# Performance work log

Measured on AMD Instinct MI355X. Metric: run time of the kernel, lower is better.

The kernel has to match this reference:

```python
import jax, jax.numpy as jnp
import numpy as np
import math

B, H, W, CV = 8, 128, 128, 256
T, CT = 77, 512
HEADS, HEAD_DIM = 8, 32
TOP_M = 5
LN_EPS = 1e-5
NORM_EPS = 1e-6
CLAMP = 2.0


def _ln(x, w, b):
    mu = jnp.mean(x, axis=-1, keepdims=True)
    var = jnp.mean(jnp.square(x - mu), axis=-1, keepdims=True)
    return (x - mu) * jax.lax.rsqrt(var + LN_EPS) * w + b


def _l2norm(x):
    n = jnp.sqrt(jnp.sum(jnp.square(x), axis=-1, keepdims=True))
    return x / jnp.maximum(n, NORM_EPS)


def setup_inputs() -> dict:
    key = jax.random.key(0)
    ks = jax.random.split(key, 12)
    s = 0.02
    return {
        "visual_features": jax.random.normal(ks[0], (B, H, W, CV), jnp.float32),
        "text_features": jax.random.normal(ks[1], (B, T, CT), jnp.float32),
        "norm1_w": jnp.ones((CV,), jnp.float32),
        "norm1_b": jnp.zeros((CV,), jnp.float32),
        "q_w": s * jax.random.normal(ks[2], (CV, CV), jnp.float32),
        "q_b": jnp.zeros((CV,), jnp.float32),
        "k_w": s * jax.random.normal(ks[3], (CT, CV), jnp.float32),
        "k_b": jnp.zeros((CV,), jnp.float32),
        "v_w": s * jax.random.normal(ks[4], (CT, CV), jnp.float32),
        "v_b": jnp.zeros((CV,), jnp.float32),
        "out_w": s * jax.random.normal(ks[5], (CV, CV), jnp.float32),
        "out_b": jnp.zeros((CV,), jnp.float32),
        "gate_w": s * jax.random.normal(ks[6], (CV, 1), jnp.float32),
        "gate_b": jnp.zeros((1,), jnp.float32),
        "logit_scale": jnp.asarray(math.log(1.0 / 0.07), jnp.float32),
        "alpha": jnp.asarray(0.1, jnp.float32),
        "norm2_w": jnp.ones((CV,), jnp.float32),
        "norm2_b": jnp.zeros((CV,), jnp.float32),
        "ffn1_w": s * jax.random.normal(ks[7], (CV, 4 * CV), jnp.float32),
        "ffn1_b": jnp.zeros((4 * CV,), jnp.float32),
        "ffn2_w": s * jax.random.normal(ks[8], (4 * CV, CV), jnp.float32),
        "ffn2_b": jnp.zeros((CV,), jnp.float32),
    }


def reference(visual_features, text_features, norm1_w, norm1_b, q_w, q_b, k_w, k_b,
              v_w, v_b, out_w, out_b, gate_w, gate_b, logit_scale, alpha,
              norm2_w, norm2_b, ffn1_w, ffn1_b, ffn2_w, ffn2_b):
    b, h, w, cv = visual_features.shape
    n = h * w
    # Pre-LN then flatten spatial dims: (B, N, Cv)
    x = _ln(visual_features, norm1_w, norm1_b).reshape(b, n, cv)
    q_full = x @ q_w + q_b                      # (B, N, Cv)
    k_full = text_features @ k_w + k_b          # (B, T, Cv)
    v_full = text_features @ v_w + v_b          # (B, T, Cv)
    # padding mask: all-zero text tokens
    pad = jnp.sum(jnp.abs(text_features), axis=-1) <= 1e-6  # (B, T)
    # cosine-normalize over FULL Cv dim, then split heads
    q = _l2norm(q_full).reshape(b, n, HEADS, HEAD_DIM)
    k = _l2norm(k_full).reshape(b, -1, HEADS, HEAD_DIM)
    v = v_full.reshape(b, -1, HEADS, HEAD_DIM)
    scale = jnp.exp(jnp.clip(logit_scale, -CLAMP, CLAMP)) / jnp.sqrt(jnp.float32(HEAD_DIM))
    sim = jnp.einsum('bnhd,bthd->bnht', q, k) * scale  # (B, N, Hh, T)
    sim = jnp.where(pad[:, None, None, :], -jnp.inf, sim)
    # top-k pruning over text tokens (threshold at k-th value; ties measure-zero)
    topv = jax.lax.top_k(sim, TOP_M)[0]
    sim = jnp.where(sim >= topv[..., -1:], sim, -jnp.inf)
    attn = jax.nn.softmax(sim, axis=-1)
    aligned = jnp.einsum('bnht,bthd->bnhd', attn, v).reshape(b, n, cv)
    aligned = aligned @ out_w + out_b
    gate = jax.nn.sigmoid(x @ gate_w + gate_b)  # (B, N, 1)
    y = x + alpha * gate * aligned
    y = _ln(y, norm2_w, norm2_b)
    ffn = jax.nn.gelu(y @ ffn1_w + ffn1_b, approximate=False) @ ffn2_w + ffn2_b
    y = y + ffn
    return y.reshape(b, h, w, cv)
```

## Files before the change

### kernel.cpp

```cpp
#include <hip/hip_runtime.h>
#include <hip/hip_bf16.h>

typedef _Float16 h16;
typedef __attribute__((ext_vector_type(8))) _Float16 halfx8;
typedef __attribute__((ext_vector_type(4))) _Float16 halfx4;
typedef __attribute__((ext_vector_type(4))) float f32x4;

__device__ __forceinline__ void gload_lds16(const void* g, void* l) {
  __builtin_amdgcn_global_load_lds((const __attribute__((address_space(1))) unsigned int*)g,
                                   (__attribute__((address_space(3))) unsigned int*)l, 16, 0, 0);
}
__device__ __forceinline__ unsigned umax_(unsigned a, unsigned b) { return a > b ? a : b; }
__device__ __forceinline__ unsigned umin_(unsigned a, unsigned b) { return a < b ? a : b; }

__device__ __forceinline__ float fast_gelu(float v) {
  float x2 = v * v;
  float w_ = v * fmaf(x2, 0.0713548163f, 1.5957691216f);
  float e = __expf(w_);
  float r = 1.f / (1.f + e);
  return v * e * r;
}

__global__ __launch_bounds__(256) void prep_kernel(
    const float* __restrict__ tf, const float* __restrict__ kw, const float* __restrict__ kb,
    const float* __restrict__ vw, const float* __restrict__ vb, const float* __restrict__ lsp,
    h16* __restrict__ ko, h16* __restrict__ vo, float* __restrict__ padf,
    const float* __restrict__ qw, const float* __restrict__ ow,
    const float* __restrict__ f1w, const float* __restrict__ f2w,
    h16* __restrict__ qwT, h16* __restrict__ owT,
    h16* __restrict__ f1T, h16* __restrict__ f2T,
    const float* __restrict__ vis, const float* __restrict__ n1w, const float* __restrict__ n1b,
    const float* __restrict__ gw, const float* __restrict__ gb,
    h16* __restrict__ x, float* __restrict__ gate)
{
  __shared__ h16 st[4 * 512];
  __shared__ float kro[4 * 256];
  __shared__ float ssc[4];
  int bid = blockIdx.x, tid = threadIdx.x;
  int lane = tid & 63, wid = tid >> 6;

  if (bid < 160) {
    int b = bid / 20, tg = bid % 20, t0 = tg * 4;
    for (int i = tid; i < 4 * 512; i += 256) {
      int tl = i >> 9, j = i & 511, t = t0 + tl;
      float v = (t < 77) ? tf[((size_t)b * 77 + t) * 512 + j] : 0.f;
      st[i] = (h16)v;
    }
    __syncthreads();
    {
      int t = t0 + wid;
      float a = 0.f;
      #pragma unroll
      for (int j = 0; j < 8; j++) a += fabsf((float)st[wid * 512 + lane + j * 64]);
      #pragma unroll
      for (int o = 32; o; o >>= 1) a += __shfl_xor(a, o);
      if (lane == 0) padf[b * 80 + t] = (a <= 1e-6f) ? -1e30f : 0.f;
    }
    int c = tid;
    float kacc[4], vacc[4];
    #pragma unroll
    for (int tl = 0; tl < 4; tl++) { kacc[tl] = kb[c]; vacc[tl] = vb[c]; }
    for (int j = 0; j < 512; j++) {
      float wkv = kw[(size_t)j * 256 + c];
      float wvv = vw[(size_t)j * 256 + c];
      #pragma unroll
      for (int tl = 0; tl < 4; tl++) {
        float xv = (float)st[tl * 512 + j];
        kacc[tl] += xv * wkv; vacc[tl] += xv * wvv;
      }
    }
    #pragma unroll
    for (int tl = 0; tl < 4; tl++) kro[tl * 256 + c] = kacc[tl] * kacc[tl];
    __syncthreads();
    {
      float s2 = kro[wid * 256 + lane] + kro[wid * 256 + lane + 64]
               + kro[wid * 256 + lane + 128] + kro[wid * 256 + lane + 192];
      #pragma unroll
      for (int o = 32; o; o >>= 1) s2 += __shfl_xor(s2, o);
      if (lane == 0) {
        float ls = lsp[0];
        float scale = __expf(fminf(fmaxf(ls, -2.f), 2.f)) * rsqrtf(32.f);
        ssc[wid] = scale / fmaxf(sqrtf(s2), 1e-6f);
      }
    }
    __syncthreads();
    int h = c >> 5, d = c & 31, g = d >> 3, e = d & 7;
    #pragma unroll
    for (int tl = 0; tl < 4; tl++) {
      int t = t0 + tl;
      int kt = t >> 4, l15 = t & 15, ln = g * 16 + l15;
      size_t koff = ((((size_t)(b * 8 + h) * 5 + kt) * 64) + ln) * 8 + e;
      size_t voff = (((size_t)(b * 8 + h) * 80) + t) * 32 + d;
      ko[koff] = (t < 77) ? (h16)(kacc[tl] * ssc[tl]) : (h16)0.f;
      vo[voff] = (t < 77) ? (h16)vacc[tl] : (h16)0.f;
    }
  } else if (bid < 2720) {
    int cb = bid - 160;
    const float* in; h16* out; int logN, K, base;
    if (cb < 256)       { in = qw;  out = qwT; logN = 8;  K = 256;  base = 0; }
    else if (cb < 512)  { in = ow;  out = owT; logN = 8;  K = 256;  base = 256; }
    else if (cb < 1536) { in = f1w; out = f1T; logN = 10; K = 256;  base = 512; }
    else                { in = f2w; out = f2T; logN = 8;  K = 1024; base = 1536; }
    int idx = (cb - base) * 256 + tid;
    int k = idx >> logN, n = idx & ((1 << logN) - 1);
    out[(size_t)n * K + k] = (h16)in[idx];
  } else {
    size_t row = (size_t)(bid - 2720) * 4 + wid;
    const float4 v = ((const float4*)(vis + row * 256))[lane];
    float s = v.x + v.y + v.z + v.w;
    float q = v.x * v.x + v.y * v.y + v.z * v.z + v.w * v.w;
    #pragma unroll
    for (int o = 32; o; o >>= 1) { s += __shfl_xor(s, o); q += __shfl_xor(q, o); }
    float mean = s * (1.f / 256.f);
    float rstd = rsqrtf(q * (1.f / 256.f) - mean * mean + 1e-5f);
    float4 wv = ((const float4*)n1w)[lane], bv = ((const float4*)n1b)[lane];
    float x0 = (v.x - mean) * rstd * wv.x + bv.x;
    float x1 = (v.y - mean) * rstd * wv.y + bv.y;
    float x2 = (v.z - mean) * rstd * wv.z + bv.z;
    float x3 = (v.w - mean) * rstd * wv.w + bv.w;
    float4 gv = ((const float4*)gw)[lane];
    float g = x0 * gv.x + x1 * gv.y + x2 * gv.z + x3 * gv.w;
    #pragma unroll
    for (int o = 32; o; o >>= 1) g += __shfl_xor(g, o);
    if (lane == 0) gate[row] = 1.f / (1.f + __expf(-(g + gb[0])));
    halfx4 o4; o4[0] = (h16)x0; o4[1] = (h16)x1; o4[2] = (h16)x2; o4[3] = (h16)x3;
    ((halfx4*)(x + row * 256))[lane] = o4;
  }
}

__global__ __launch_bounds__(256) void gemmQA_kernel(const h16* __restrict__ A,
    const h16* __restrict__ Wt, const float* __restrict__ bias,
    const h16* __restrict__ kk,
    const h16* __restrict__ vv,
    const float* __restrict__ padf,
    h16* __restrict__ outp)
{
  __shared__ char sA[8192];
  __shared__ char sB[32768];
  int m0 = blockIdx.x * 64;
  int tid = threadIdx.x, lane = tid & 63, wid = tid >> 6;
  int wn = wid;
  int l15 = lane & 15, l4 = lane >> 4, xk = l15 & 7;
  f32x4 acc[4][4];
  #pragma unroll
  for (int a = 0; a < 4; a++)
    #pragma unroll
    for (int b2 = 0; b2 < 4; b2++) acc[a][b2] = (f32x4){0.f, 0.f, 0.f, 0.f};
  const size_t sa = 512;
  int srow = lane >> 3;
  int scol = ((lane & 7) ^ srow) * 16;
  const char* Ab = (const char*)A + (size_t)m0 * sa + scol;
  const char* Bb = (const char*)Wt + scol;
  for (int k0 = 0; k0 < 256; k0 += 64) {
    #pragma unroll
    for (int cc = 0; cc < 2; cc++) {
      int ch = wid * 2 + cc;
      gload_lds16(Ab + (size_t)(ch * 8 + srow) * sa + k0 * 2, sA + ch * 1024);
    }
    #pragma unroll
    for (int cc = 0; cc < 8; cc++) {
      int ch = wid * 8 + cc;
      gload_lds16(Bb + (size_t)(ch * 8 + srow) * sa + k0 * 2, sB + ch * 1024);
    }
    asm volatile("s_waitcnt vmcnt(0)" ::: "memory");
    __syncthreads();
    #pragma unroll
    for (int ks = 0; ks < 2; ks++) {
      halfx8 af[4], bf[4];
      #pragma unroll
      for (int f = 0; f < 4; f++) {
        af[f] = *(const halfx8*)(sA + (f * 16 + l15) * 128 + (((ks * 4 + l4) ^ xk) * 16));
        bf[f] = *(const halfx8*)(sB + (wn * 64 + f * 16 + l15) * 128 + (((ks * 4 + l4) ^ xk) * 16));
      }
      #pragma unroll
      for (int fm = 0; fm < 4; fm++)
        #pragma unroll
        for (int fn = 0; fn < 4; fn++)
          acc[fm][fn] = __builtin_amdgcn_mfma_f32_16x16x32_f16(af[fm], bf[fn], acc[fm][fn], 0, 0, 0);
    }
    __syncthreads();
  }
  float bv[4];
  #pragma unroll
  for (int fn = 0; fn < 4; fn++) bv[fn] = bias[wn * 64 + fn * 16 + l15];
  float ps[4][4];
  #pragma unroll
  for (int fm = 0; fm < 4; fm++)
    #pragma unroll
    for (int r = 0; r < 4; r++) {
      float s = 0.f;
      #pragma unroll
      for (int fn = 0; fn < 4; fn++) {
        float v = acc[fm][fn][r] + bv[fn];
        acc[fm][fn][r] = v;
        s += v * v;
      }
      ps[fm][r] = s;
    }
  #pragma unroll
  for (int o = 1; o <= 8; o <<= 1)
    #pragma unroll
    for (int fm = 0; fm < 4; fm++)
      #pragma unroll
      for (int r = 0; r < 4; r++) ps[fm][r] += __shfl_xor(ps[fm][r], o);
  if (l15 == 0) {
    #pragma unroll
    for (int fm = 0; fm < 4; fm++)
      #pragma unroll
      for (int r = 0; r < 4; r++)
        ((float*)sA)[(fm * 16 + l4 * 4 + r) * 4 + wn] = ps[fm][r];
  }
  __syncthreads();
  #pragma unroll
  for (int fm = 0; fm < 4; fm++)
    #pragma unroll
    for (int r = 0; r < 4; r++) {
      const float* p = (const float*)sA + (fm * 16 + l4 * 4 + r) * 4;
      float S = p[0] + p[1] + p[2] + p[3];
      float sc = 1.f / fmaxf(sqrtf(S), 1e-6f);
      int row = fm * 16 + l4 * 4 + r;
      #pragma unroll
      for (int fn = 0; fn < 4; fn++) {
        int col = wn * 64 + fn * 16 + l15;
        ((h16*)(sB + row * 512 + (((col >> 3) ^ (row & 7)) * 16)))[col & 7] =
            (h16)(acc[fm][fn][r] * sc);
      }
    }
  __syncthreads();

  {
    int bx = blockIdx.x;
    int g = l4;
    int b = bx >> 8;
    size_t qrow = (size_t)bx * 64 + wid * 16 + l15;
    int base4 = g * 4;
    float pad4[5][4];
    #pragma unroll
    for (int kt = 0; kt < 5; kt++) {
      float4 p4 = *(const float4*)&padf[b * 80 + kt * 16 + base4];
      pad4[kt][0] = p4.x; pad4[kt][1] = p4.y; pad4[kt][2] = p4.z; pad4[kt][3] = p4.w;
    }
    const char* qsrc = sB + (wid * 16 + l15) * 512;
    int rk = l15 & 7;
    h16* op = &outp[qrow * 256 + g * 8];
    #pragma unroll 2
    for (int h = 0; h < 8; h++) {
      int ho = h * 32;
      halfx8 qf = *(const halfx8*)(qsrc + (((h * 4 + l4) ^ rk) * 16));
      const h16* kph = kk + (((size_t)(b * 8 + h) * 5) * 64 + lane) * 8;
      const h16* vph = vv + ((size_t)(b * 8 + h) * 80) * 32 + g * 8;
      f32x4 acc5[5];
      #pragma unroll
      for (int kt = 0; kt < 5; kt++) {
        halfx8 kf = *(const halfx8*)(kph + kt * 512);
        acc5[kt] = __builtin_amdgcn_mfma_f32_16x16x32_f16(kf, qf, (f32x4){0.f, 0.f, 0.f, 0.f}, 0, 0, 0);
      }
      unsigned pv0 = 0u, pv1 = 0u, pv2 = 0u, pv3 = 0u, pv4 = 0u;
      #pragma unroll
      for (int kt = 0; kt < 5; kt++) {
        #pragma unroll
        for (int r = 0; r < 4; r++) {
          float s = acc5[kt][r] + pad4[kt][r];
          int bi = __float_as_int(s);
          unsigned u = ((unsigned)(bi ^ ((bi >> 31) | (int)0x80000000)) & 0xFFFFFF80u)
                     | (unsigned)(base4 + kt * 16 + r);
          unsigned a;
          a = umax_(pv0, u); u = umin_(pv0, u); pv0 = a;
          a = umax_(pv1, u); u = umin_(pv1, u); pv1 = a;
          a = umax_(pv2, u); u = umin_(pv2, u); pv2 = a;
          a = umax_(pv3, u); u = umin_(pv3, u); pv3 = a;
          pv4 = umax_(pv4, u);
        }
      }
      #pragma unroll
      for (int mrd = 0; mrd < 2; mrd++) {
        int msk = mrd ? 32 : 16;
        unsigned b0 = (unsigned)__shfl_xor((int)pv0, msk);
        unsigned b1 = (unsigned)__shfl_xor((int)pv1, msk);
        unsigned b2 = (unsigned)__shfl_xor((int)pv2, msk);
        unsigned b3 = (unsigned)__shfl_xor((int)pv3, msk);
        unsigned b4 = (unsigned)__shfl_xor((int)pv4, msk);
        unsigned c0 = umax_(pv0, b0);
        unsigned c1 = umax_(umax_(umin_(pv0, b0), pv1), b1);
        unsigned c2 = umax_(umax_(umin_(pv0, b1), umin_(pv1, b0)), umax_(pv2, b2));
        unsigned c3 = umax_(umax_(umax_(umin_(pv0, b2), umin_(pv1, b1)), umin_(pv2, b0)), umax_(pv3, b3));
        unsigned c4 = umax_(umax_(umax_(umin_(pv0, b3), umin_(pv1, b2)),
                                  umax_(umin_(pv2, b1), umin_(pv3, b0))), umax_(pv4, b4));
        pv0 = c0; pv1 = c1; pv2 = c2; pv3 = c3; pv4 = c4;
      }
      unsigned pvs[5] = {pv0, pv1, pv2, pv3, pv4};
      float pw[5]; int ti[5]; float den = 0.f;
      #pragma unroll
      for (int k = 0; k < 5; k++) {
        unsigned u = pvs[k];
        int sg = ((int)u) >> 31;
        float tv = __int_as_float(u ^ (0x80000000u | (unsigned)~sg));
        ti[k] = (int)(u & 0x7Fu);
        pw[k] = __expf(tv);
        den += pw[k];
      }
      float inv = 1.f / den;
      halfx8 o8 = {};
      #pragma unroll
      for (int k = 0; k < 5; k++) {
        h16 ph = (h16)(pw[k] * inv);
        halfx8 v = *(const halfx8*)(vph + ti[k] * 32);
        halfx8 p8 = {ph, ph, ph, ph, ph, ph, ph, ph};
        o8 = o8 + p8 * v;
      }
      *(halfx8*)(op + ho) = o8;
    }
  }
}

__global__ __launch_bounds__(256) void gemmO_kernel(const h16* __restrict__ A,
    const h16* __restrict__ Wt, const float* __restrict__ ob,
    const h16* __restrict__ x, const float* __restrict__ gate,
    const float* __restrict__ alphap, const float* __restrict__ w2,
    const float* __restrict__ b2, h16* __restrict__ outp)
{
  __shared__ char sA[8192];
  __shared__ char sB[32768];
  int m0 = blockIdx.x * 64;
  int tid = threadIdx.x, lane = tid & 63, wid = tid >> 6;
  int wn = wid;
  int l15 = lane & 15, l4 = lane >> 4, xk = l15 & 7;
  f32x4 acc[4][4];
  #pragma unroll
  for (int a = 0; a < 4; a++)
    #pragma unroll
    for (int b2_ = 0; b2_ < 4; b2_++) acc[a][b2_] = (f32x4){0.f, 0.f, 0.f, 0.f};
  const size_t sa = 512;
  int srow = lane >> 3;
  int scol = ((lane & 7) ^ srow) * 16;
  const char* Ab = (const char*)A + (size_t)m0 * sa + scol;
  const char* Bb = (const char*)Wt + scol;
  for (int k0 = 0; k0 < 256; k0 += 64) {
    #pragma unroll
    for (int cc = 0; cc < 2; cc++) {
      int ch = wid * 2 + cc;
      gload_lds16(Ab + (size_t)(ch * 8 + srow) * sa + k0 * 2, sA + ch * 1024);
    }
    #pragma unroll
    for (int cc = 0; cc < 8; cc++) {
      int ch = wid * 8 + cc;
      gload_lds16(Bb + (size_t)(ch * 8 + srow) * sa + k0 * 2, sB + ch * 1024);
    }
    asm volatile("s_waitcnt vmcnt(0)" ::: "memory");
    __syncthreads();
    #pragma unroll
    for (int ks = 0; ks < 2; ks++) {
      halfx8 af[4], bf[4];
      #pragma unroll
      for (int f = 0; f < 4; f++) {
        af[f] = *(const halfx8*)(sA + (f * 16 + l15) * 128 + (((ks * 4 + l4) ^ xk) * 16));
        bf[f] = *(const halfx8*)(sB + (wn * 64 + f * 16 + l15) * 128 + (((ks * 4 + l4) ^ xk) * 16));
      }
      #pragma unroll
      for (int fm = 0; fm < 4; fm++)
        #pragma unroll
        for (int fn = 0; fn < 4; fn++)
          acc[fm][fn] = __builtin_amdgcn_mfma_f32_16x16x32_f16(af[fm], bf[fn], acc[fm][fn], 0, 0, 0);
    }
    __syncthreads();
  }
  float bv[4], w2v[4], b2v[4];
  #pragma unroll
  for (int fn = 0; fn < 4; fn++) {
    int col = wn * 64 + fn * 16 + l15;
    bv[fn] = ob[col]; w2v[fn] = w2[col]; b2v[fn] = b2[col];
  }
  float al = alphap[0];
  float s1[4][4], s2[4][4];
  #pragma unroll
  for (int fm = 0; fm < 4; fm++)
    #pragma unroll
    for (int r = 0; r < 4; r++) {
      size_t row = (size_t)(m0 + fm * 16 + l4 * 4 + r);
      float ga = al * gate[row];
      float a1 = 0.f, a2 = 0.f;
      #pragma unroll
      for (int fn = 0; fn < 4; fn++) {
        float v = acc[fm][fn][r] + bv[fn];
        float xv = (float)x[row * 256 + wn * 64 + fn * 16 + l15];
        float y = xv + ga * v;
        acc[fm][fn][r] = y;
        a1 += y; a2 += y * y;
      }
      s1[fm][r] = a1; s2[fm][r] = a2;
    }
  #pragma unroll
  for (int o = 1; o <= 8; o <<= 1)
    #pragma unroll
    for (int fm = 0; fm < 4; fm++)
      #pragma unroll
      for (int r = 0; r < 4; r++) {
        s1[fm][r] += __shfl_xor(s1[fm][r], o);
        s2[fm][r] += __shfl_xor(s2[fm][r], o);
      }
  if (l15 == 0) {
    #pragma unroll
    for (int fm = 0; fm < 4; fm++)
      #pragma unroll
      for (int r = 0; r < 4; r++) {
        int rr = fm * 16 + l4 * 4 + r;
        ((float*)sA)[rr * 8 + wn * 2 + 0] = s1[fm][r];
        ((float*)sA)[rr * 8 + wn * 2 + 1] = s2[fm][r];
      }
  }
  __syncthreads();
  #pragma unroll
  for (int fm = 0; fm < 4; fm++)
    #pragma unroll
    for (int r = 0; r < 4; r++) {
      int rr = fm * 16 + l4 * 4 + r;
      const float* p = (const float*)sA + rr * 8;
      float S1 = p[0] + p[2] + p[4] + p[6];
      float S2 = p[1] + p[3] + p[5] + p[7];
      float mean = S1 * (1.f / 256.f);
      float var = S2 * (1.f / 256.f) - mean * mean;
      float rstd = rsqrtf(var + 1e-5f);
      size_t row = (size_t)(m0 + rr);
      #pragma unroll
      for (int fn = 0; fn < 4; fn++) {
        float y = acc[fm][fn][r];
        outp[row * 256 + wn * 64 + fn * 16 + l15] =
            (h16)((y - mean) * rstd * w2v[fn] + b2v[fn]);
      }
    }
}

__device__ __forceinline__ void ffn_stage_w1(const h16* __restrict__ w1t,
                                             int c, char* dW1, int tid, int wid)
{
  #pragma unroll
  for (int j = 0; j < 4; j++) {
    int i = j * 512 + tid;
    int r = i >> 5, g = i & 31;
    gload_lds16(w1t + (size_t)(c * 64 + r) * 256 + ((g ^ (r & 7)) * 8),
                dW1 + (j * 512 + wid * 64) * 16);
  }
}
__device__ __forceinline__ void ffn_stage_w2(const h16* __restrict__ w2t,
                                             int c, char* dW2, int tid, int wid)
{
  #pragma unroll
  for (int j = 0; j < 4; j++) {
    int i = j * 512 + tid;
    int r = i >> 3, g = i & 7;
    gload_lds16(w2t + (size_t)r * 1024 + c * 64 + ((g ^ (r & 7)) * 8),
                dW2 + (j * 512 + wid * 64) * 16);
  }
}

__global__ __launch_bounds__(512, 2) void ffn_fused_kernel(
    const h16* __restrict__ y2g, const h16* __restrict__ w1t, const float* __restrict__ b1,
    const h16* __restrict__ w2t, const float* __restrict__ b2, float* __restrict__ outp)
{
  __shared__ char smem[163840];
  float* sE = (float*)smem;

  int m0 = blockIdx.x * 128;
  int tid = threadIdx.x, lane = tid & 63, wid = tid >> 6;
  int l15 = lane & 15, l4 = lane >> 4;
  int wm1 = wid >> 1, wn1 = wid & 1;
  int wm2 = wid >> 2, wn2 = wid & 3;

  halfx8 afy[2][8];
  #pragma unroll
  for (int fm = 0; fm < 2; fm++) {
    size_t row = (size_t)(m0 + wm1 * 32 + fm * 16 + l15);
    #pragma unroll
    for (int ks = 0; ks < 8; ks++)
      afy[fm][ks] = *(const halfx8*)&y2g[row * 256 + ks * 32 + l4 * 8];
  }

  f32x4 acc2[4][4];
  #pragma unroll
  for (int a = 0; a < 4; a++)
    #pragma unroll
    for (int b_ = 0; b_ < 4; b_++) acc2[a][b_] = (f32x4){0.f, 0.f, 0.f, 0.f};

  ffn_stage_w1(w1t, 0, smem, tid, wid);
  float4 b1v[2];
  b1v[0] = *(const float4*)&b1[wn1 * 32 + l4 * 4];
  b1v[1] = *(const float4*)&b1[wn1 * 32 + 16 + l4 * 4];
  asm volatile("s_waitcnt vmcnt(0)" ::: "memory");
  __builtin_amdgcn_s_barrier();
  asm volatile("" ::: "memory");

  for (int c = 0; c < 16; c++) {
    int buf = c & 1;
    char* sW1c = smem + buf * 32768;
    if (c < 15) ffn_stage_w1(w1t, c + 1, smem + (buf ^ 1) * 32768, tid, wid);
    ffn_stage_w2(w2t, c, smem + 65536 + buf * 32768, tid, wid);
    float4 nb0 = {0.f, 0.f, 0.f, 0.f}, nb1 = {0.f, 0.f, 0.f, 0.f};
    if (c < 15) {
      nb0 = *(const float4*)&b1[(c + 1) * 64 + wn1 * 32 + l4 * 4];
      nb1 = *(const float4*)&b1[(c + 1) * 64 + wn1 * 32 + 16 + l4 * 4];
    }

    f32x4 a1[2][2];
    #pragma unroll
    for (int a = 0; a < 2; a++)
      #pragma unroll
      for (int b_ = 0; b_ < 2; b_++) a1[a][b_] = (f32x4){0.f, 0.f, 0.f, 0.f};
    __builtin_amdgcn_s_setprio(1);
    #pragma unroll
    for (int ks = 0; ks < 8; ks++) {
      #pragma unroll
      for (int fc = 0; fc < 2; fc++) {
        int nrow = wn1 * 32 + fc * 16 + l15;
        halfx8 bf = *(const halfx8*)(sW1c + (size_t)nrow * 512 + (((ks * 4 + l4) ^ (nrow & 7)) * 16));
        #pragma unroll
        for (int fm = 0; fm < 2; fm++)
          a1[fm][fc] = __builtin_amdgcn_mfma_f32_16x16x32_f16(bf, afy[fm][ks], a1[fm][fc], 0, 0, 0);
      }
    }
    __builtin_amdgcn_s_setprio(0);

    {
      char* sHc = smem + 131072 + buf * 16384;
      #pragma unroll
      for (int fm = 0; fm < 2; fm++) {
        int row = wm1 * 32 + fm * 16 + l15;
        int sx = (row & 7) << 1;
        #pragma unroll
        for (int fc = 0; fc < 2; fc++) {
          int slot = wn1 * 8 + fc * 4 + l4;
          float4 bb = b1v[fc];
          halfx4 hv;
          hv[0] = (h16)fast_gelu(a1[fm][fc][0] + bb.x);
          hv[1] = (h16)fast_gelu(a1[fm][fc][1] + bb.y);
          hv[2] = (h16)fast_gelu(a1[fm][fc][2] + bb.z);
          hv[3] = (h16)fast_gelu(a1[fm][fc][3] + bb.w);
          *(halfx4*)(sHc + row * 128 + ((slot ^ sx) * 8)) = hv;
        }
      }
    }

    if (c > 0) {
      char* sHp = smem + 131072 + (buf ^ 1) * 16384;
      char* sW2p = smem + 65536 + (buf ^ 1) * 32768;
      __builtin_amdgcn_s_setprio(1);
      #pragma unroll
      for (int ks = 0; ks < 2; ks++) {
        halfx8 ah[4], bw[4];
        #pragma unroll
        for (int f = 0; f < 4; f++) {
          int hrow = wm2 * 64 + f * 16 + l15;
          ah[f] = *(const halfx8*)(sHp + hrow * 128 + (((ks * 8 + l4 * 2) ^ ((hrow & 7) << 1)) * 8));
          int wrow = wn2 * 64 + f * 16 + l15;
          bw[f] = *(const halfx8*)(sW2p + (size_t)wrow * 128 + (((ks * 4 + l4) ^ (wrow & 7)) * 16));
        }
        #pragma unroll
        for (int fm = 0; fm < 4; fm++)
          #pragma unroll
          for (int fn = 0; fn < 4; fn++)
            acc2[fm][fn] = __builtin_amdgcn_mfma_f32_16x16x32_f16(ah[fm], bw[fn], acc2[fm][fn], 0, 0, 0);
      }
      __builtin_amdgcn_s_setprio(0);
    }

    asm volatile("s_waitcnt lgkmcnt(0)" ::: "memory");
    asm volatile("s_waitcnt vmcnt(0)" ::: "memory");
    __builtin_amdgcn_s_barrier();
    asm volatile("" ::: "memory");
    b1v[0] = nb0; b1v[1] = nb1;
  }

  {
    char* sHp = smem + 131072 + 16384;
    char* sW2p = smem + 65536 + 32768;
    __builtin_amdgcn_s_setprio(1);
    #pragma unroll
    for (int ks = 0; ks < 2; ks++) {
      halfx8 ah[4], bw[4];
      #pragma unroll
      for (int f = 0; f < 4; f++) {
        int hrow = wm2 * 64 + f * 16 + l15;
        ah[f] = *(const halfx8*)(sHp + hrow * 128 + (((ks * 8 + l4 * 2) ^ ((hrow & 7) << 1)) * 8));
        int wrow = wn2 * 64 + f * 16 + l15;
        bw[f] = *(const halfx8*)(sW2p + (size_t)wrow * 128 + (((ks * 4 + l4) ^ (wrow & 7)) * 16));
      }
      #pragma unroll
      for (int fm = 0; fm < 4; fm++)
        #pragma unroll
        for (int fn = 0; fn < 4; fn++)
          acc2[fm][fn] = __builtin_amdgcn_mfma_f32_16x16x32_f16(ah[fm], bw[fn], acc2[fm][fn], 0, 0, 0);
    }
    __builtin_amdgcn_s_setprio(0);
  }

  int rowl = tid >> 3, cg = tid & 7;
  #pragma unroll
  for (int half = 0; half < 2; half++) {
    if (wm2 == half) {
      #pragma unroll
      for (int fm = 0; fm < 4; fm++)
        #pragma unroll
        for (int fn = 0; fn < 4; fn++)
          #pragma unroll
          for (int r = 0; r < 4; r++)
            sE[(fm * 16 + l4 * 4 + r) * 264 + wn2 * 64 + fn * 16 + l15] = acc2[fm][fn][r];
    }
    __syncthreads();
    size_t grow = (size_t)(m0 + half * 64 + rowl);
    #pragma unroll
    for (int k = 0; k < 8; k++) {
      int c0 = cg * 4 + k * 32;
      float4 v = *(float4*)&sE[rowl * 264 + c0];
      halfx4 rv = *(const halfx4*)&y2g[grow * 256 + c0];
      float4 bb = *(const float4*)&b2[c0];
      float4 o;
      o.x = v.x + (float)rv[0] + bb.x;
      o.y = v.y + (float)rv[1] + bb.y;
      o.z = v.z + (float)rv[2] + bb.z;
      o.w = v.w + (float)rv[3] + bb.w;
      *(float4*)&outp[grow * 256 + c0] = o;
    }
    __syncthreads();
  }
}

extern "C" void kernel_launch(void* const* d_in, const int* in_sizes, int n_in,
                              void* d_out, int out_size, void* d_ws, size_t ws_size,
                              hipStream_t stream)
{
  const float* vis = (const float*)d_in[0];
  const float* tf  = (const float*)d_in[1];
  const float* n1w = (const float*)d_in[2];
  const float* n1b = (const float*)d_in[3];
  const float* qw  = (const float*)d_in[4];
  const float* qb  = (const float*)d_in[5];
  const float* kw  = (const float*)d_in[6];
  const float* kb  = (const float*)d_in[7];
  const float* vw  = (const float*)d_in[8];
  const float* vb  = (const float*)d_in[9];
  const float* ow  = (const float*)d_in[10];
  const float* ob  = (const float*)d_in[11];
  const float* gw  = (const float*)d_in[12];
  const float* gb  = (const float*)d_in[13];
  const float* ls  = (const float*)d_in[14];
  const float* al  = (const float*)d_in[15];
  const float* n2w = (const float*)d_in[16];
  const float* n2b = (const float*)d_in[17];
  const float* f1w = (const float*)d_in[18];
  const float* f1b = (const float*)d_in[19];
  const float* f2w = (const float*)d_in[20];
  const float* f2b = (const float*)d_in[21];

  char* ws = (char*)d_ws;
  const size_t MB_ = 1024ull * 1024ull;
  h16*  kS   = (h16*)(ws + 0 * MB_);
  h16*  vS   = (h16*)(ws + 1 * MB_);
  float* padf = (float*)(ws + 2 * MB_);
  float* gate = (float*)(ws + 3 * MB_);
  h16*  qwT  = (h16*)(ws + 4 * MB_);
  h16*  owT  = (h16*)(ws + 5 * MB_);
  h16*  f1T  = (h16*)(ws + 6 * MB_);
  h16*  f2T  = (h16*)(ws + 7 * MB_);
  h16*  xh   = (h16*)(ws + 16 * MB_);
  h16*  qh   = (h16*)(ws + 80 * MB_);
  h16*  alg  = (h16*)(ws + 144 * MB_);

  prep_kernel<<<35488, 256, 0, stream>>>(
      tf, kw, kb, vw, vb, ls, kS, vS, padf,
      qw, ow, f1w, f2w, qwT, owT, f1T, f2T,
      vis, n1w, n1b, gw, gb, xh, gate);

  gemmQA_kernel<<<2048, 256, 0, stream>>>(xh, qwT, qb, kS, vS, padf, qh);

  gemmO_kernel<<<2048, 256, 0, stream>>>(qh, owT, ob, xh, gate, al, n2w, n2b, alg);

  ffn_fused_kernel<<<1024, 512, 0, stream>>>(alg, f1T, f1b, f2T, f2b, (float*)d_out);
}
```

Measured before the change: 478.6 us.

## Fuse Q-projection/attention kernel with output projection and LayerNorm kernel

Merges the Q GEMM + top-k attention kernel with the out-projection + gate residual + LN2 kernel into one launch. The per-head aligned outputs stay in registers (o8s) and are written into LDS as the A operand of the out-projection GEMM, so the intermediate aligned tensor never makes the round trip through global memory. This saves one launch and roughly 32 MB of fp16 traffic. The cost is higher register pressure from holding eight halfx8 values plus fully unrolling the head loop, which may reduce occupancy.

Result: slower. 490.5 us (+2.5%).

```diff
diff --git a/kernel.cpp b/kernel.cpp
--- a/kernel.cpp
+++ b/kernel.cpp
@@ -128,12 +128,16 @@
   }
 }
 
-__global__ __launch_bounds__(256) void gemmQA_kernel(const h16* __restrict__ A,
+__global__ __launch_bounds__(256) void gemmQAO_kernel(const h16* __restrict__ A,
     const h16* __restrict__ Wt, const float* __restrict__ bias,
     const h16* __restrict__ kk,
     const h16* __restrict__ vv,
     const float* __restrict__ padf,
-    h16* __restrict__ outp)
+    const h16* __restrict__ Ot,
+    const float* __restrict__ ob,
+    const h16* __restrict__ x, const float* __restrict__ gate,
+    const float* __restrict__ alphap, const float* __restrict__ w2,
+    const float* __restrict__ b2, h16* __restrict__ outp)
 {
   __shared__ char sA[8192];
   __shared__ char sB[32768];
@@ -145,7 +149,7 @@
   #pragma unroll
   for (int a = 0; a < 4; a++)
     #pragma unroll
-    for (int b2 = 0; b2 < 4; b2++) acc[a][b2] = (f32x4){0.f, 0.f, 0.f, 0.f};
+    for (int b2_ = 0; b2_ < 4; b2_++) acc[a][b2_] = (f32x4){0.f, 0.f, 0.f, 0.f};
   const size_t sa = 512;
   int srow = lane >> 3;
   int scol = ((lane & 7) ^ srow) * 16;
@@ -228,12 +232,10 @@
     }
   __syncthreads();
 
+  halfx8 o8s[8];
   {
-    int bx = blockIdx.x;
-    int g = l4;
-    int b = bx >> 8;
-    size_t qrow = (size_t)bx * 64 + wid * 16 + l15;
-    int base4 = g * 4;
+    int b = blockIdx.x >> 8;
+    int base4 = l4 * 4;
     float pad4[5][4];
     #pragma unroll
     for (int kt = 0; kt < 5; kt++) {
@@ -242,13 +244,11 @@
     }
     const char* qsrc = sB + (wid * 16 + l15) * 512;
     int rk = l15 & 7;
-    h16* op = &outp[qrow * 256 + g * 8];
-    #pragma unroll 2
+    #pragma unroll
     for (int h = 0; h < 8; h++) {
-      int ho = h * 32;
       halfx8 qf = *(const halfx8*)(qsrc + (((h * 4 + l4) ^ rk) * 16));
       const h16* kph = kk + (((size_t)(b * 8 + h) * 5) * 64 + lane) * 8;
-      const h16* vph = vv + ((size_t)(b * 8 + h) * 80) * 32 + g * 8;
+      const h16* vph = vv + ((size_t)(b * 8 + h) * 80) * 32 + l4 * 8;
       f32x4 acc5[5];
       #pragma unroll
       for (int kt = 0; kt < 5; kt++) {
@@ -277,14 +277,14 @@
         int msk = mrd ? 32 : 16;
         unsigned b0 = (unsigned)__shfl_xor((int)pv0, msk);
         unsigned b1 = (unsigned)__shfl_xor((int)pv1, msk);
-        unsigned b2 = (unsigned)__shfl_xor((int)pv2, msk);
+        unsigned b2_ = (unsigned)__shfl_xor((int)pv2, msk);
         unsigned b3 = (unsigned)__shfl_xor((int)pv3, msk);
         unsigned b4 = (unsigned)__shfl_xor((int)pv4, msk);
         unsigned c0 = umax_(pv0, b0);
         unsigned c1 = umax_(umax_(umin_(pv0, b0), pv1), b1);
-        unsigned c2 = umax_(umax_(umin_(pv0, b1), umin_(pv1, b0)), umax_(pv2, b2));
-        unsigned c3 = umax_(umax_(umax_(umin_(pv0, b2), umin_(pv1, b1)), umin_(pv2, b0)), umax_(pv3, b3));
-        unsigned c4 = umax_(umax_(umax_(umin_(pv0, b3), umin_(pv1, b2)),
+        unsigned c2 = umax_(umax_(umin_(pv0, b1), umin_(pv1, b0)), umax_(pv2, b2_));
+        unsigned c3 = umax_(umax_(umax_(umin_(pv0, b2_), umin_(pv1, b1)), umin_(pv2, b0)), umax_(pv3, b3));
+        unsigned c4 = umax_(umax_(umax_(umin_(pv0, b3), umin_(pv1, b2_)),
                                   umax_(umin_(pv2, b1), umin_(pv3, b0))), umax_(pv4, b4));
         pv0 = c0; pv1 = c1; pv2 = c2; pv3 = c3; pv4 = c4;
       }
@@ -308,67 +308,58 @@
         halfx8 p8 = {ph, ph, ph, ph, ph, ph, ph, ph};
         o8 = o8 + p8 * v;
       }
-      *(halfx8*)(op + ho) = o8;
-    }
-  }
-}
-
-__global__ __launch_bounds__(256) void gemmO_kernel(const h16* __restrict__ A,
-    const h16* __restrict__ Wt, const float* __restrict__ ob,
-    const h16* __restrict__ x, const float* __restrict__ gate,
-    const float* __restrict__ alphap, const float* __restrict__ w2,
-    const float* __restrict__ b2, h16* __restrict__ outp)
-{
-  __shared__ char sA[8192];
-  __shared__ char sB[32768];
-  int m0 = blockIdx.x * 64;
-  int tid = threadIdx.x, lane = tid & 63, wid = tid >> 6;
-  int wn = wid;
-  int l15 = lane & 15, l4 = lane >> 4, xk = l15 & 7;
-  f32x4 acc[4][4];
+      o8s[h] = o8;
+    }
+  }
+
+  asm volatile("" ::: "memory");
+  __builtin_amdgcn_s_barrier();
+  asm volatile("" ::: "memory");
+
+  f32x4 acc2[4][4];
   #pragma unroll
   for (int a = 0; a < 4; a++)
     #pragma unroll
-    for (int b2_ = 0; b2_ < 4; b2_++) acc[a][b2_] = (f32x4){0.f, 0.f, 0.f, 0.f};
-  const size_t sa = 512;
-  int srow = lane >> 3;
-  int scol = ((lane & 7) ^ srow) * 16;
-  const char* Ab = (const char*)A + (size_t)m0 * sa + scol;
-  const char* Bb = (const char*)Wt + scol;
-  for (int k0 = 0; k0 < 256; k0 += 64) {
-    #pragma unroll
-    for (int cc = 0; cc < 2; cc++) {
-      int ch = wid * 2 + cc;
-      gload_lds16(Ab + (size_t)(ch * 8 + srow) * sa + k0 * 2, sA + ch * 1024);
-    }
-    #pragma unroll
-    for (int cc = 0; cc < 8; cc++) {
-      int ch = wid * 8 + cc;
-      gload_lds16(Bb + (size_t)(ch * 8 + srow) * sa + k0 * 2, sB + ch * 1024);
-    }
-    asm volatile("s_waitcnt vmcnt(0)" ::: "memory");
-    __syncthreads();
-    #pragma unroll
-    for (int ks = 0; ks < 2; ks++) {
-      halfx8 af[4], bf[4];
-      #pragma unroll
-      for (int f = 0; f < 4; f++) {
-        af[f] = *(const halfx8*)(sA + (f * 16 + l15) * 128 + (((ks * 4 + l4) ^ xk) * 16));
-        bf[f] = *(const halfx8*)(sB + (wn * 64 + f * 16 + l15) * 128 + (((ks * 4 + l4) ^ xk) * 16));
-      }
-      #pragma unroll
-      for (int fm = 0; fm < 4; fm++)
-        #pragma unroll
-        for (int fn = 0; fn < 4; fn++)
-          acc[fm][fn] = __builtin_amdgcn_mfma_f32_16x16x32_f16(af[fm], bf[fn], acc[fm][fn], 0, 0, 0);
-    }
-    __syncthreads();
-  }
-  float bv[4], w2v[4], b2v[4];
+    for (int b_ = 0; b_ < 4; b_++) acc2[a][b_] = (f32x4){0.f, 0.f, 0.f, 0.f};
+  const char* Ob = (const char*)Ot + scol;
+  {
+    int arow = wid * 16 + l15;
+    int ark = arow & 7;
+    for (int k0 = 0; k0 < 256; k0 += 64) {
+      #pragma unroll
+      for (int ks = 0; ks < 2; ks++)
+        *(halfx8*)(sA + arow * 128 + (((ks * 4 + l4) ^ ark) * 16)) = o8s[(k0 >> 5) + ks];
+      #pragma unroll
+      for (int cc = 0; cc < 8; cc++) {
+        int ch = wid * 8 + cc;
+        gload_lds16(Ob + (size_t)(ch * 8 + srow) * sa + k0 * 2, sB + ch * 1024);
+      }
+      asm volatile("s_waitcnt vmcnt(0)" ::: "memory");
+      asm volatile("s_waitcnt lgkmcnt(0)" ::: "memory");
+      __syncthreads();
+      #pragma unroll
+      for (int ks = 0; ks < 2; ks++) {
+        halfx8 af[4], bf[4];
+        #pragma unroll
+        for (int f = 0; f < 4; f++) {
+          af[f] = *(const halfx8*)(sA + (f * 16 + l15) * 128 + (((ks * 4 + l4) ^ xk) * 16));
+          bf[f] = *(const halfx8*)(sB + (wn * 64 + f * 16 + l15) * 128 + (((ks * 4 + l4) ^ xk) * 16));
+        }
+        #pragma unroll
+        for (int fm = 0; fm < 4; fm++)
+          #pragma unroll
+          for (int fn = 0; fn < 4; fn++)
+            acc2[fm][fn] = __builtin_amdgcn_mfma_f32_16x16x32_f16(af[fm], bf[fn], acc2[fm][fn], 0, 0, 0);
+      }
+      __syncthreads();
+    }
+  }
+
+  float bv2[4], w2v[4], b2v[4];
   #pragma unroll
   for (int fn = 0; fn < 4; fn++) {
     int col = wn * 64 + fn * 16 + l15;
-    bv[fn] = ob[col]; w2v[fn] = w2[col]; b2v[fn] = b2[col];
+    bv2[fn] = ob[col]; w2v[fn] = w2[col]; b2v[fn] = b2[col];
   }
   float al = alphap[0];
   float s1[4][4], s2[4][4];
@@ -381,10 +372,10 @@
       float a1 = 0.f, a2 = 0.f;
       #pragma unroll
       for (int fn = 0; fn < 4; fn++) {
-        float v = acc[fm][fn][r] + bv[fn];
+        float v = acc2[fm][fn][r] + bv2[fn];
         float xv = (float)x[row * 256 + wn * 64 + fn * 16 + l15];
         float y = xv + ga * v;
-        acc[fm][fn][r] = y;
+        acc2[fm][fn][r] = y;
         a1 += y; a2 += y * y;
       }
       s1[fm][r] = a1; s2[fm][r] = a2;
@@ -423,7 +414,7 @@
       size_t row = (size_t)(m0 + rr);
       #pragma unroll
       for (int fn = 0; fn < 4; fn++) {
-        float y = acc[fm][fn][r];
+        float y = acc2[fm][fn][r];
         outp[row * 256 + wn * 64 + fn * 16 + l15] =
             (h16)((y - mean) * rstd * w2v[fn] + b2v[fn]);
       }
@@ -661,7 +652,6 @@
   h16*  f1T  = (h16*)(ws + 6 * MB_);
   h16*  f2T  = (h16*)(ws + 7 * MB_);
   h16*  xh   = (h16*)(ws + 16 * MB_);
-  h16*  qh   = (h16*)(ws + 80 * MB_);
   h16*  alg  = (h16*)(ws + 144 * MB_);
 
   prep_kernel<<<35488, 256, 0, stream>>>(
@@ -669,9 +659,8 @@
       qw, ow, f1w, f2w, qwT, owT, f1T, f2T,
       vis, n1w, n1b, gw, gb, xh, gate);
 
-  gemmQA_kernel<<<2048, 256, 0, stream>>>(xh, qwT, qb, kS, vS, padf, qh);
-
-  gemmO_kernel<<<2048, 256, 0, stream>>>(qh, owT, ob, xh, gate, al, n2w, n2b, alg);
+  gemmQAO_kernel<<<2048, 256, 0, stream>>>(xh, qwT, qb, kS, vS, padf,
+                                           owT, ob, xh, gate, al, n2w, n2b, alg);
 
   ffn_fused_kernel<<<1024, 512, 0, stream>>>(alg, f1T, f1b, f2T, f2b, (float*)d_out);
 }
```
